# Kernel optimization log

Measured on AMD Instinct MI355X. Metric: run time of the kernel, lower is better.

Reference implementation:

```python
import jax, jax.numpy as jnp
import numpy as np

B, C, H, W = 8, 128, 128, 128
WS, NH = 4, 8
HD = C // NH
SCALE = HD ** -0.5
HG, WG = H // WS, W // WS
G, N = HG * WG, WS * WS


def conv2d(x, w, b, padding=0, groups=1):
    out = jax.lax.conv_general_dilated(
        x, w, (1, 1), [(padding, padding)] * 2,
        dimension_numbers=('NCHW', 'OIHW', 'NCHW'),
        feature_group_count=groups)
    return out + b[None, :, None, None]


def dsc(x, dw_w, dw_b, pw_w, pw_b):
    # depthwise 3x3 (groups=C) then pointwise 1x1
    h = conv2d(x, dw_w, dw_b, padding=1, groups=x.shape[1])
    return conv2d(h, pw_w, pw_b)


def _window(t):
    # (B,C,H,W) -> (B,G,NH,N,HD) exactly as torch reshape/permute
    t = t.reshape(B, NH, HD, HG, WS, WG, WS)
    return t.transpose(0, 3, 5, 1, 4, 6, 2).reshape(B, G, NH, N, HD)


def setup_inputs() -> dict:
    key = jax.random.key(0)
    ks = jax.random.split(key, 32)
    s = 0.02
    Cr = max(C // 8, 1)
    d = {
        'x': jax.random.normal(ks[0], (B, C, H, W), jnp.float32),
        'y': jax.random.normal(ks[1], (B, C, H, W), jnp.float32),
        'ca_w1': jax.random.normal(ks[2], (Cr, 2 * C, 1, 1)) * s,
        'ca_b1': jnp.zeros((Cr,)),
        'ca_w2': jax.random.normal(ks[3], (2 * C, Cr, 1, 1)) * s,
        'ca_b2': jnp.zeros((2 * C,)),
        'final_w': jax.random.normal(ks[4], (C, 3 * C, 1, 1)) * s,
        'final_b': jnp.zeros((C,)),
        'bn_g': jnp.ones((C,)),
        'bn_b': jnp.zeros((C,)),
        'bn_m': jnp.zeros((C,)),
        'bn_v': jnp.ones((C,)),
    }
    for i, name in enumerate(['q', 'k', 'v', 'proj']):
        d[name + '_dw_w'] = jax.random.normal(ks[5 + 4 * i], (C, 1, 3, 3)) * s
        d[name + '_dw_b'] = jnp.zeros((C,))
        d[name + '_pw_w'] = jax.random.normal(ks[6 + 4 * i], (C, C, 1, 1)) * s
        d[name + '_pw_b'] = jnp.zeros((C,))
    return d


def reference(x, y, ca_w1, ca_b1, ca_w2, ca_b2,
              q_dw_w, q_dw_b, q_pw_w, q_pw_b,
              k_dw_w, k_dw_b, k_pw_w, k_pw_b,
              v_dw_w, v_dw_b, v_pw_w, v_pw_b,
              proj_dw_w, proj_dw_b, proj_pw_w, proj_pw_b,
              final_w, final_b, bn_g, bn_b, bn_m, bn_v):
    element_wise = x * y
    concat = jnp.concatenate([x, y], axis=1)  # (B,2C,H,W)
    # channel attention (squeeze-excite)
    pooled = concat.mean(axis=(2, 3), keepdims=True)
    h = jax.nn.relu(conv2d(pooled, ca_w1, ca_b1))
    ca = jax.nn.sigmoid(conv2d(h, ca_w2, ca_b2))
    attended = concat * ca
    x_att, y_att = attended[:, :C], attended[:, C:]
    # windowed cross-attention: q from y_att, k/v from x_att
    q = _window(dsc(y_att, q_dw_w, q_dw_b, q_pw_w, q_pw_b))
    k = _window(dsc(x_att, k_dw_w, k_dw_b, k_pw_w, k_pw_b))
    v = _window(dsc(x_att, v_dw_w, v_dw_b, v_pw_w, v_pw_b))
    attn = jnp.einsum('bgnqd,bgnkd->bgnqk', q, k) * SCALE
    attn = jax.nn.softmax(attn, axis=-1)
    out = jnp.einsum('bgnqk,bgnkd->bgnqd', attn, v)  # (B,G,NH,N,HD)
    out = out.transpose(0, 1, 3, 2, 4).reshape(B, HG, WG, WS, WS, C)
    out = out.transpose(0, 1, 3, 2, 4, 5).reshape(B, H, W, C).transpose(0, 3, 1, 2)
    cross = dsc(out, proj_dw_w, proj_dw_b, proj_pw_w, proj_pw_b)
    fused = jnp.concatenate([element_wise, y_att, cross], axis=1)
    z = conv2d(fused, final_w, final_b)
    # BatchNorm in eval mode with running stats
    inv = jax.lax.rsqrt(bn_v + 1e-5)
    z = (z - bn_m[None, :, None, None]) * (inv * bn_g)[None, :, None, None] + bn_b[None, :, None, None]
    return jax.nn.relu(z)
```

## Files before the change

### kernel.cpp

```cpp
#include <hip/hip_runtime.h>

typedef __attribute__((ext_vector_type(8))) short short8;
typedef __attribute__((ext_vector_type(4))) float f32x4;
typedef __attribute__((ext_vector_type(2))) unsigned u32x2;
typedef __attribute__((ext_vector_type(4))) unsigned u32x4;

static constexpr int C_ = 128, H_ = 128, W_ = 128;
static constexpr int HW_ = H_ * W_;
static constexpr int CHW_ = C_ * HW_;

__device__ __forceinline__ unsigned short f2b(float f) {
  union { float f; unsigned u; } cv; cv.f = f;
  unsigned r = cv.u + 0x7FFFu + ((cv.u >> 16) & 1u);
  return (unsigned short)(r >> 16);
}
__device__ __forceinline__ float b2f(unsigned short h) {
  union { unsigned u; float f; } cv; cv.u = ((unsigned)h) << 16;
  return cv.f;
}
__device__ __forceinline__ float uasf(unsigned u) {
  union { unsigned u; float f; } cv; cv.u = u; return cv.f;
}
__device__ __forceinline__ int swzo(int pos, int byteInRow) {
  return pos * 256 + (byteInRow ^ ((pos & 7) << 4));
}

__global__ __launch_bounds__(256) void k_pool(const float* __restrict__ x,
                                              const float* __restrict__ y,
                                              float* __restrict__ sums) {
  int blk = blockIdx.x;
  int b = blk >> 8, c = blk & 255;
  const float* src = (c < C_) ? (x + (size_t)b * CHW_ + (size_t)c * HW_)
                              : (y + (size_t)b * CHW_ + (size_t)(c - C_) * HW_);
  const float4* s4 = (const float4*)src;
  float acc = 0.f;
  for (int i = threadIdx.x; i < HW_ / 4; i += 256) {
    float4 v = s4[i];
    acc += v.x + v.y + v.z + v.w;
  }
  for (int off = 32; off; off >>= 1) acc += __shfl_down(acc, off, 64);
  __shared__ float red[4];
  int lane = threadIdx.x & 63, wv = threadIdx.x >> 6;
  if (lane == 0) red[wv] = acc;
  __syncthreads();
  if (threadIdx.x == 0) sums[blk] = red[0] + red[1] + red[2] + red[3];
}

__global__ __launch_bounds__(256) void k_ca(const float* __restrict__ sums,
                                            const float* __restrict__ w1,
                                            const float* __restrict__ b1,
                                            const float* __restrict__ w2,
                                            const float* __restrict__ b2,
                                            float* __restrict__ ca) {
  int b = blockIdx.x;
  __shared__ float pooled[256];
  __shared__ float hb[16];
  int t = threadIdx.x;
  pooled[t] = sums[b * 256 + t] * (1.f / 16384.f);
  __syncthreads();
  if (t < 16) {
    float s = b1[t];
    for (int j = 0; j < 256; ++j) s += w1[t * 256 + j] * pooled[j];
    hb[t] = fmaxf(s, 0.f);
  }
  __syncthreads();
  float s = b2[t];
  for (int r = 0; r < 16; ++r) s += w2[t * 16 + r] * hb[r];
  ca[b * 256 + t] = 1.f / (1.f + __expf(-s));
}

__global__ __launch_bounds__(128) void k_prep(
    const float* __restrict__ qpw, const float* __restrict__ kpw,
    const float* __restrict__ vpw,
    const float* __restrict__ fw, const float* __restrict__ fb,
    const float* __restrict__ ppw, const float* __restrict__ ppb,
    const float* __restrict__ cab,
    unsigned short* __restrict__ Wb, unsigned short* __restrict__ W2b,
    float* __restrict__ bc) {
  int blk = blockIdx.x, c = threadIdx.x;
  if (blk < 768) {
    int mat = blk >> 7, o = blk & 127;
    float v = 0.f;
    if (mat == 0) v = qpw[o * 128 + c];
    else if (mat == 1) v = kpw[o * 128 + c];
    else if (mat == 2) v = vpw[o * 128 + c];
    else if (mat == 3) {
      float a = 0.f;
      for (int m = 0; m < 128; ++m) a += fw[o * 384 + 256 + m] * ppw[m * 128 + c];
      v = a;
      if (c == 0) {
        float bb = fb[o];
        for (int m = 0; m < 128; ++m) bb += fw[o * 384 + 256 + m] * ppb[m];
        bc[o] = bb;
      }
    } else if (mat == 4) v = fw[o * 384 + c];
    else v = 0.f;
    Wb[((size_t)mat << 14) + o * 128 + c] = f2b(v);
  } else {
    int bb = (blk - 768) >> 7, o = blk & 127;
    W2b[((size_t)bb << 14) + o * 128 + c] =
        f2b(fw[o * 384 + 128 + c] * cab[bb * 256 + 128 + c]);
  }
}

__global__ __launch_bounds__(512, 4) void k_qkv_attn(
    const float* __restrict__ x, const float* __restrict__ y,
    const float* __restrict__ cab,
    const float* __restrict__ qdw, const float* __restrict__ qdb,
    const float* __restrict__ kdw, const float* __restrict__ kdb,
    const float* __restrict__ vdw, const float* __restrict__ vdb,
    const unsigned short* __restrict__ Wqkv,
    const float* __restrict__ qpb, const float* __restrict__ kpb,
    const float* __restrict__ vpb,
    unsigned short* __restrict__ outb) {
  __shared__ __align__(16) char lds[81920];
  constexpr int QS = 0, KS = 16384, VT = 32768, A1 = 49152, A2 = 65536;
  constexpr int HA = 16384, SCR = 49152, OS = 65536;

  const int t = threadIdx.x;
  const int l = t & 63;
  const int w = t >> 6;
  const int lm = l & 15, g = l >> 4;
  const int bs = ((blockIdx.x & 7) << 8) | (blockIdx.x >> 3);
  const int b = bs >> 8, tr = bs & 255;
  const int y0 = (tr >> 3) << 2, x0 = (tr & 7) << 4;
  const int ct = t & 127, rowt = t >> 7;
  unsigned short* hal = (unsigned short*)(lds + HA);

  auto halo_issue = [&](const float* src, f32x4 (*hv)[6]) {
    #pragma unroll
    for (int tk = 0; tk < 2; ++tk) {
      int task = t + tk * 512;
      bool tv = task < 768;
      int c = task & 127, hr = task >> 7;
      int gy = y0 - 1 + hr;
      bool rowok = tv && ((unsigned)gy < 128u);
      const float* rsrc = src + (size_t)c * HW_ + gy * W_;
      #pragma unroll
      for (int ck = 0; ck < 6; ++ck) {
        int gxc = x0 - 4 + 4 * ck;
        bool ok = rowok && ((unsigned)gxc < 125u);
        hv[tk][ck] = ok ? *(const f32x4*)(rsrc + gxc) : f32x4{0.f, 0.f, 0.f, 0.f};
      }
    }
  };
  auto halo_write = [&](const f32x4 (*hv)[6]) {
    #pragma unroll
    for (int tk = 0; tk < 2; ++tk) {
      int task = t + tk * 512;
      if (task < 768) {
        int base = ((task >> 7) * 128 + (task & 127)) * 18;
        const float* f = (const float*)hv[tk];
        #pragma unroll
        for (int e = 0; e < 9; ++e) {
          unsigned u = (unsigned)f2b(f[2 * e + 3]) |
                       ((unsigned)f2b(f[2 * e + 4]) << 16);
          *(unsigned*)(hal + base + 2 * e) = u;
        }
      }
    }
  };

  auto dw_one = [&](const float* wdw, const float* bdw, const float* cas,
                    int aOff) {
    const float* wp = wdw + ct * 9;
    float wr[9];
    #pragma unroll
    for (int k2 = 0; k2 < 9; ++k2) wr[k2] = wp[k2];
    float cam = cas[ct], bb = bdw[ct];
    float o[16];
    #pragma unroll
    for (int px = 0; px < 16; ++px) o[px] = 0.f;
    #pragma unroll
    for (int rr = 0; rr < 3; ++rr) {
      int base = ((rowt + rr) * 128 + ct) * 18;
      unsigned rp[9];
      #pragma unroll
      for (int e = 0; e < 9; ++e) rp[e] = *(const unsigned*)(hal + base + 2 * e);
      float rv[18];
      #pragma unroll
      for (int e = 0; e < 9; ++e) {
        rv[2 * e] = uasf(rp[e] << 16);
        rv[2 * e + 1] = uasf(rp[e] & 0xffff0000u);
      }
      #pragma unroll
      for (int px = 0; px < 16; ++px)
        o[px] += rv[px] * wr[3 * rr] + rv[px + 1] * wr[3 * rr + 1] +
                 rv[px + 2] * wr[3 * rr + 2];
    }
    #pragma unroll
    for (int px = 0; px < 16; ++px)
      *(unsigned short*)(lds + aOff + swzo(rowt * 16 + px, 2 * ct)) =
          f2b(o[px] * cam + bb);
  };
  auto dw_kv = [&](const float* kw, const float* kb2, const float* vw,
                   const float* vb2, const float* cas) {
    const float* kp = kw + ct * 9;
    const float* vp = vw + ct * 9;
    float wk[9], wv2[9];
    #pragma unroll
    for (int k2 = 0; k2 < 9; ++k2) { wk[k2] = kp[k2]; wv2[k2] = vp[k2]; }
    float cam = cas[ct], kbb = kb2[ct], vbb = vb2[ct];
    float ok[16], ov[16];
    #pragma unroll
    for (int px = 0; px < 16; ++px) { ok[px] = 0.f; ov[px] = 0.f; }
    #pragma unroll
    for (int rr = 0; rr < 3; ++rr) {
      int base = ((rowt + rr) * 128 + ct) * 18;
      unsigned rp[9];
      #pragma unroll
      for (int e = 0; e < 9; ++e) rp[e] = *(const unsigned*)(hal + base + 2 * e);
      float rv[18];
      #pragma unroll
      for (int e = 0; e < 9; ++e) {
        rv[2 * e] = uasf(rp[e] << 16);
        rv[2 * e + 1] = uasf(rp[e] & 0xffff0000u);
      }
      #pragma unroll
      for (int px = 0; px < 16; ++px) {
        ok[px] += rv[px] * wk[3 * rr] + rv[px + 1] * wk[3 * rr + 1] +
                  rv[px + 2] * wk[3 * rr + 2];
        ov[px] += rv[px] * wv2[3 * rr] + rv[px + 1] * wv2[3 * rr + 1] +
                  rv[px + 2] * wv2[3 * rr + 2];
      }
    }
    #pragma unroll
    for (int px = 0; px < 16; ++px) {
      int so = swzo(rowt * 16 + px, 2 * ct);
      *(unsigned short*)(lds + A1 + so) = f2b(ok[px] * cam + kbb);
      *(unsigned short*)(lds + A2 + so) = f2b(ov[px] * cam + vbb);
    }
  };

  const int mtile = w & 3, nbase = (w >> 2) * 64;

  auto gemm_qk = [&](int aOff, const unsigned short* Wm, const float* bias,
                     int dstOff) {
    f32x4 acc[4];
    #pragma unroll
    for (int nt = 0; nt < 4; ++nt) acc[nt] = f32x4{0.f, 0.f, 0.f, 0.f};
    #pragma unroll
    for (int ks = 0; ks < 4; ++ks) {
      short8 wf[4];
      #pragma unroll
      for (int nt = 0; nt < 4; ++nt)
        wf[nt] = *(const short8*)(Wm + (nbase + nt * 16 + lm) * 128 +
                                  ks * 32 + g * 8);
      short8 a = *(const short8*)(lds + aOff +
                   swzo(mtile * 16 + lm, ks * 64 + g * 16));
      #pragma unroll
      for (int nt = 0; nt < 4; ++nt)
        acc[nt] = __builtin_amdgcn_mfma_f32_16x16x32_bf16(a, wf[nt], acc[nt], 0, 0, 0);
    }
    #pragma unroll
    for (int nt = 0; nt < 4; ++nt) {
      int ch = nbase + nt * 16 + lm;
      float bv = bias[ch];
      #pragma unroll
      for (int r2 = 0; r2 < 4; ++r2) {
        int pos = mtile * 16 + g * 4 + r2;
        *(unsigned short*)(lds + dstOff + swzo(pos, 2 * ch)) =
            f2b(acc[nt][r2] + bv);
      }
    }
  };
  auto gemm_v = [&](int aOff, const unsigned short* Wm, const float* bias) {
    f32x4 acc[4];
    #pragma unroll
    for (int nt = 0; nt < 4; ++nt) acc[nt] = f32x4{0.f, 0.f, 0.f, 0.f};
    #pragma unroll
    for (int ks = 0; ks < 4; ++ks) {
      short8 wf[4];
      #pragma unroll
      for (int nt = 0; nt < 4; ++nt)
        wf[nt] = *(const short8*)(Wm + (nbase + nt * 16 + lm) * 128 +
                                  ks * 32 + g * 8);
      short8 a = *(const short8*)(lds + aOff +
                   swzo(mtile * 16 + lm, ks * 64 + g * 16));
      #pragma unroll
      for (int nt = 0; nt < 4; ++nt)
        acc[nt] = __builtin_amdgcn_mfma_f32_16x16x32_bf16(a, wf[nt], acc[nt], 0, 0, 0);
    }
    #pragma unroll
    for (int nt = 0; nt < 4; ++nt) {
      int ch = nbase + nt * 16 + lm;
      float bv = bias[ch];
      int col = (g * 16 + mtile * 4) ^ ((ch & 7) << 3);
      unsigned lo = (unsigned)f2b(acc[nt][0] + bv) |
                    ((unsigned)f2b(acc[nt][1] + bv) << 16);
      unsigned hi = (unsigned)f2b(acc[nt][2] + bv) |
                    ((unsigned)f2b(acc[nt][3] + bv) << 16);
      *(u32x2*)(lds + VT + ch * 128 + 2 * col) = u32x2{lo, hi};
    }
  };

  const float* cax = cab + b * 256;
  const float* cay = cax + 128;

  f32x4 hy[2][6], hx[2][6];
  halo_issue(y + (size_t)b * CHW_, hy);
  halo_issue(x + (size_t)b * CHW_, hx);
  halo_write(hy);
  __syncthreads();
  dw_one(qdw, qdb, cay, A1);
  __syncthreads();
  halo_write(hx);
  gemm_qk(A1, Wqkv, qpb, QS);
  __syncthreads();
  dw_kv(kdw, kdb, vdw, vdb, cax);
  __syncthreads();
  gemm_qk(A1, Wqkv + 16384, kpb, KS);
  gemm_v(A2, Wqkv + 32768, vpb);
  __syncthreads();

  {
    const int h = w;
    const int chb = h * 32;
    char* scr = lds + SCR + w * 512;
    const short8 zz = {};
    #pragma unroll
    for (int wi = 0; wi < 4; ++wi) {
      int rowp = (lm >> 2) * 16 + wi * 4 + (lm & 3);
      short8 av = zz, bv = zz;
      if (g < 2) {
        av = *(const short8*)(lds + KS + swzo(rowp, chb + g * 16));
        bv = *(const short8*)(lds + QS + swzo(rowp, chb + g * 16));
      }
      f32x4 st = __builtin_amdgcn_mfma_f32_16x16x32_bf16(
          av, bv, f32x4{0.f, 0.f, 0.f, 0.f}, 0, 0, 0);
      float s0 = st[0] * 0.25f, s1 = st[1] * 0.25f,
            s2 = st[2] * 0.25f, s3 = st[3] * 0.25f;
      float mx = fmaxf(fmaxf(s0, s1), fmaxf(s2, s3));
      mx = fmaxf(mx, __shfl_xor(mx, 16, 64));
      mx = fmaxf(mx, __shfl_xor(mx, 32, 64));
      float e0 = __expf(s0 - mx), e1 = __expf(s1 - mx),
            e2 = __expf(s2 - mx), e3 = __expf(s3 - mx);
      float sm = e0 + e1 + e2 + e3;
      sm += __shfl_xor(sm, 16, 64);
      sm += __shfl_xor(sm, 32, 64);
      float rl = 1.f / sm;
      unsigned p0 = (unsigned)f2b(e0 * rl) | ((unsigned)f2b(e1 * rl) << 16);
      unsigned p1 = (unsigned)f2b(e2 * rl) | ((unsigned)f2b(e3 * rl) << 16);
      *(u32x2*)(scr + lm * 32 + g * 8) = u32x2{p0, p1};
      short8 pb2 = zz, va = zz;
      if (g < 2) {
        pb2 = *(const short8*)(scr + lm * 32 + g * 16);
        int ch = h * 16 + lm;
        va = *(const short8*)(lds + VT + ch * 128 +
                              2 * ((wi * 16 + g * 8) ^ ((ch & 7) << 3)));
      }
      f32x4 ot = __builtin_amdgcn_mfma_f32_16x16x32_bf16(
          va, pb2, f32x4{0.f, 0.f, 0.f, 0.f}, 0, 0, 0);
      unsigned o0 = (unsigned)f2b(ot[0]) | ((unsigned)f2b(ot[1]) << 16);
      unsigned o1 = (unsigned)f2b(ot[2]) | ((unsigned)f2b(ot[3]) << 16);
      *(u32x2*)(lds + OS + swzo(rowp, chb + g * 8)) = u32x2{o0, o1};
    }
  }
  __syncthreads();
  {
    unsigned short* dst = outb + (size_t)b * CHW_ + (size_t)ct * HW_ +
                          (y0 + rowt) * W_ + x0;
    unsigned v[8];
    #pragma unroll
    for (int j = 0; j < 8; ++j) {
      unsigned lo = *(const unsigned short*)(lds + OS + swzo(rowt * 16 + 2 * j, 2 * ct));
      unsigned hi = *(const unsigned short*)(lds + OS + swzo(rowt * 16 + 2 * j + 1, 2 * ct));
      v[j] = lo | (hi << 16);
    }
    *(u32x4*)(dst) = u32x4{v[0], v[1], v[2], v[3]};
    *(u32x4*)(dst + 8) = u32x4{v[4], v[5], v[6], v[7]};
  }
}

__global__ __launch_bounds__(512, 4) void k_final(
    const float* __restrict__ x, const float* __restrict__ y,
    const unsigned short* __restrict__ outb,
    const float* __restrict__ pdw, const float* __restrict__ pdb,
    const unsigned short* __restrict__ W3,
    const unsigned short* __restrict__ W2b,
    const float* __restrict__ bc,
    const float* __restrict__ bng, const float* __restrict__ bnb,
    const float* __restrict__ bnm, const float* __restrict__ bnv,
    float* __restrict__ outp) {
  __shared__ __align__(16) char lds[50176];
  constexpr int A1 = 0, HA = 16384;

  const int t = threadIdx.x, l = t & 63, w = t >> 6;
  const int lm = l & 15, g = l >> 4;
  const int bs = ((blockIdx.x & 7) << 8) | (blockIdx.x >> 3);
  const int b = bs >> 8, tr = bs & 255;
  const int y0 = (tr >> 3) << 2, x0 = (tr & 7) << 4;
  const int ct = t & 127, rowt = t >> 7;
  unsigned short* hal = (unsigned short*)(lds + HA);
  const int mtile = w & 3, nbase = (w >> 2) * 64;

  f32x4 acc[4];
  #pragma unroll
  for (int nt = 0; nt < 4; ++nt) acc[nt] = f32x4{0.f, 0.f, 0.f, 0.f};

  auto gemm_acc = [&](const unsigned short* Wm) {
    #pragma unroll
    for (int ks = 0; ks < 4; ++ks) {
      short8 wf[4];
      #pragma unroll
      for (int nt = 0; nt < 4; ++nt)
        wf[nt] = *(const short8*)(Wm + (nbase + nt * 16 + lm) * 128 +
                                  ks * 32 + g * 8);
      short8 a = *(const short8*)(lds + A1 +
                   swzo(mtile * 16 + lm, ks * 64 + g * 16));
      #pragma unroll
      for (int nt = 0; nt < 4; ++nt)
        acc[nt] = __builtin_amdgcn_mfma_f32_16x16x32_bf16(a, wf[nt], acc[nt], 0, 0, 0);
    }
  };

  const size_t gbase = (size_t)b * CHW_ + (size_t)ct * HW_ +
                       (size_t)(y0 + rowt) * W_ + x0;
  f32x4 xv[4], yv[4];
  #pragma unroll
  for (int e = 0; e < 4; ++e) {
    xv[e] = *(const f32x4*)(x + gbase + 4 * e);
    yv[e] = *(const f32x4*)(y + gbase + 4 * e);
  }
  unsigned hreg[2][10];
  #pragma unroll
  for (int tk = 0; tk < 2; ++tk) {
    int task = t + tk * 512;
    bool tv = task < 768;
    int c = task & 127, hr = task >> 7;
    int gy = y0 - 1 + hr;
    bool rowok = tv && ((unsigned)gy < 128u);
    const unsigned short* hsrc = outb + (size_t)b * CHW_ + (size_t)c * HW_ + gy * W_;
    #pragma unroll
    for (int e = 0; e < 10; ++e) {
      int gx0 = x0 - 2 + 2 * e;
      bool okp = rowok && ((unsigned)gx0 < 127u);
      hreg[tk][e] = okp ? *(const unsigned*)(hsrc + gx0) : 0u;
    }
  }
  #pragma unroll
  for (int e = 0; e < 4; ++e)
    #pragma unroll
    for (int j = 0; j < 4; ++j)
      *(unsigned short*)(lds + A1 + swzo(rowt * 16 + 4 * e + j, 2 * ct)) =
          f2b(xv[e][j] * yv[e][j]);
  #pragma unroll
  for (int tk = 0; tk < 2; ++tk) {
    int task = t + tk * 512;
    if (task < 768) {
      int base = ((task >> 7) * 128 + (task & 127)) * 22;
      #pragma unroll
      for (int e = 0; e < 10; ++e)
        *(unsigned*)(hal + base + 2 * e) = hreg[tk][e];
    }
  }
  __syncthreads();
  gemm_acc(W3 + 16384);
  __syncthreads();
  #pragma unroll
  for (int e = 0; e < 4; ++e)
    #pragma unroll
    for (int j = 0; j < 4; ++j)
      *(unsigned short*)(lds + A1 + swzo(rowt * 16 + 4 * e + j, 2 * ct)) =
          f2b(yv[e][j]);
  __syncthreads();
  gemm_acc(W2b + ((size_t)b << 14));
  __syncthreads();
  {
    const float* wp = pdw + ct * 9;
    float wr[9];
    #pragma unroll
    for (int k2 = 0; k2 < 9; ++k2) wr[k2] = wp[k2];
    float bb = pdb[ct];
    float o[16];
    #pragma unroll
    for (int px = 0; px < 16; ++px) o[px] = 0.f;
    #pragma unroll
    for (int rr = 0; rr < 3; ++rr) {
      int base = ((rowt + rr) * 128 + ct) * 22;
      unsigned rp[10];
      #pragma unroll
      for (int e = 0; e < 10; ++e) rp[e] = *(const unsigned*)(hal + base + 2 * e);
      float rv[20];
      #pragma unroll
      for (int e = 0; e < 10; ++e) {
        rv[2 * e] = uasf(rp[e] << 16);
        rv[2 * e + 1] = uasf(rp[e] & 0xffff0000u);
      }
      #pragma unroll
      for (int px = 0; px < 16; ++px)
        o[px] += rv[px + 1] * wr[3 * rr] + rv[px + 2] * wr[3 * rr + 1] +
                 rv[px + 3] * wr[3 * rr + 2];
    }
    #pragma unroll
    for (int px = 0; px < 16; ++px)
      *(unsigned short*)(lds + A1 + swzo(rowt * 16 + px, 2 * ct)) =
          f2b(o[px] + bb);
  }
  __syncthreads();
  gemm_acc(W3);
  float* fst = (float*)(lds + HA);
  #pragma unroll
  for (int nt = 0; nt < 4; ++nt) {
    int ch = nbase + nt * 16 + lm;
    float zb = bc[ch];
    float inv = rsqrtf(bnv[ch] + 1e-5f);
    float gsc = inv * bng[ch];
    float mm = bnm[ch], ab = bnb[ch];
    #pragma unroll
    for (int r2 = 0; r2 < 4; ++r2) {
      int pos = mtile * 16 + g * 4 + r2;
      float z = acc[nt][r2] + zb;
      z = (z - mm) * gsc + ab;
      fst[pos * 130 + ch] = fmaxf(z, 0.f);
    }
  }
  __syncthreads();
  #pragma unroll
  for (int e4 = 0; e4 < 4; ++e4) {
    f32x4 ov;
    #pragma unroll
    for (int j = 0; j < 4; ++j) ov[j] = fst[(rowt * 16 + e4 * 4 + j) * 130 + ct];
    *(f32x4*)(outp + gbase + 4 * e4) = ov;
  }
}

extern "C" void kernel_launch(void* const* d_in, const int* in_sizes, int n_in,
                              void* d_out, int out_size, void* d_ws, size_t ws_size,
                              hipStream_t stream) {
  const float* x       = (const float*)d_in[0];
  const float* y       = (const float*)d_in[1];
  const float* ca_w1   = (const float*)d_in[2];
  const float* ca_b1   = (const float*)d_in[3];
  const float* ca_w2   = (const float*)d_in[4];
  const float* ca_b2   = (const float*)d_in[5];
  const float* final_w = (const float*)d_in[6];
  const float* final_b = (const float*)d_in[7];
  const float* bn_g    = (const float*)d_in[8];
  const float* bn_b    = (const float*)d_in[9];
  const float* bn_m    = (const float*)d_in[10];
  const float* bn_v    = (const float*)d_in[11];
  const float* q_dw_w  = (const float*)d_in[12];
  const float* q_dw_b  = (const float*)d_in[13];
  const float* q_pw_w  = (const float*)d_in[14];
  const float* q_pw_b  = (const float*)d_in[15];
  const float* k_dw_w  = (const float*)d_in[16];
  const float* k_dw_b  = (const float*)d_in[17];
  const float* k_pw_w  = (const float*)d_in[18];
  const float* k_pw_b  = (const float*)d_in[19];
  const float* v_dw_w  = (const float*)d_in[20];
  const float* v_dw_b  = (const float*)d_in[21];
  const float* v_pw_w  = (const float*)d_in[22];
  const float* v_pw_b  = (const float*)d_in[23];
  const float* p_dw_w  = (const float*)d_in[24];
  const float* p_dw_b  = (const float*)d_in[25];
  const float* p_pw_w  = (const float*)d_in[26];
  const float* p_pw_b  = (const float*)d_in[27];

  char* ws = (char*)d_ws;
  float* sums = (float*)(ws + 0);
  float* cab  = (float*)(ws + 8192);
  unsigned short* Wqkv = (unsigned short*)(ws + 16384);
  unsigned short* W3   = Wqkv + 3 * 16384;
  float* bc   = (float*)(ws + 212992);
  unsigned short* W2b  = (unsigned short*)(ws + 213504);
  unsigned short* outb = (unsigned short*)(ws + (1 << 20));

  k_pool<<<2048, 256, 0, stream>>>(x, y, sums);
  k_ca<<<8, 256, 0, stream>>>(sums, ca_w1, ca_b1, ca_w2, ca_b2, cab);
  k_prep<<<1792, 128, 0, stream>>>(q_pw_w, k_pw_w, v_pw_w, final_w, final_b,
                                   p_pw_w, p_pw_b, cab, Wqkv, W2b, bc);
  k_qkv_attn<<<2048, 512, 0, stream>>>(x, y, cab,
      q_dw_w, q_dw_b, k_dw_w, k_dw_b, v_dw_w, v_dw_b,
      Wqkv, q_pw_b, k_pw_b, v_pw_b, outb);
  k_final<<<2048, 512, 0, stream>>>(x, y, outb,
      p_dw_w, p_dw_b, W3, W2b, bc,
      bn_g, bn_b, bn_m, bn_v, (float*)d_out);
}
```

Measured before the change: 360.9 us.

## Drop LDS halo staging and reuse LDS buffers to raise occupancy

The depthwise convolutions in the QKV-attention kernel now read their 3x3 neighbourhoods straight from global memory into registers instead of staging a bf16 halo tile in LDS. A-fragments are loaded into registers so the GEMM outputs can overwrite their own source buffers, and the attention output is held in registers until all waves finish. Together these shrink LDS from 80KB to 52KB, and launch bounds are raised to 6 waves per SIMD on both kernels. The cost is redundant global or L2 reads (each row is fetched three times), losing the overlap of x and y halo loads, extra barriers, and tighter register limits that may cause spills.

```diff
diff --git a/kernel.cpp b/kernel.cpp
--- a/kernel.cpp
+++ b/kernel.cpp
@@ -103,7 +103,7 @@
   }
 }
 
-__global__ __launch_bounds__(512, 4) void k_qkv_attn(
+__global__ __launch_bounds__(512, 6) void k_qkv_attn(
     const float* __restrict__ x, const float* __restrict__ y,
     const float* __restrict__ cab,
     const float* __restrict__ qdw, const float* __restrict__ qdb,
@@ -113,9 +113,11 @@
     const float* __restrict__ qpb, const float* __restrict__ kpb,
     const float* __restrict__ vpb,
     unsigned short* __restrict__ outb) {
-  __shared__ __align__(16) char lds[81920];
-  constexpr int QS = 0, KS = 16384, VT = 32768, A1 = 49152, A2 = 65536;
-  constexpr int HA = 16384, SCR = 49152, OS = 65536;
+  __shared__ __align__(16) char lds[53248];
+  constexpr int QS = 0, OS = 0;
+  constexpr int AK = 16384, KS = 16384;
+  constexpr int AV = 32768, VT = 32768;
+  constexpr int SCR = 49152;
 
   const int t = threadIdx.x;
   const int l = t & 63;
@@ -125,117 +127,85 @@
   const int b = bs >> 8, tr = bs & 255;
   const int y0 = (tr >> 3) << 2, x0 = (tr & 7) << 4;
   const int ct = t & 127, rowt = t >> 7;
-  unsigned short* hal = (unsigned short*)(lds + HA);
-
-  auto halo_issue = [&](const float* src, f32x4 (*hv)[6]) {
-    #pragma unroll
-    for (int tk = 0; tk < 2; ++tk) {
-      int task = t + tk * 512;
-      bool tv = task < 768;
-      int c = task & 127, hr = task >> 7;
-      int gy = y0 - 1 + hr;
-      bool rowok = tv && ((unsigned)gy < 128u);
-      const float* rsrc = src + (size_t)c * HW_ + gy * W_;
+  const int mtile = w & 3, nbase = (w >> 2) * 64;
+
+  auto dw_direct = [&](const float* src, const float* wdw,
+                       const float* bdw, const float* cas, int aOff) {
+    const float* wp = wdw + ct * 9;
+    const float* rbase = src + (size_t)ct * HW_;
+    float o[16];
+    #pragma unroll
+    for (int px = 0; px < 16; ++px) o[px] = 0.f;
+    #pragma unroll
+    for (int rr = 0; rr < 3; ++rr) {
+      int gy = y0 + rowt - 1 + rr;
+      bool rowok = (unsigned)gy < 128u;
+      f32x4 rx[6];
       #pragma unroll
       for (int ck = 0; ck < 6; ++ck) {
-        int gxc = x0 - 4 + 4 * ck;
-        bool ok = rowok && ((unsigned)gxc < 125u);
-        hv[tk][ck] = ok ? *(const f32x4*)(rsrc + gxc) : f32x4{0.f, 0.f, 0.f, 0.f};
-      }
-    }
-  };
-  auto halo_write = [&](const f32x4 (*hv)[6]) {
-    #pragma unroll
-    for (int tk = 0; tk < 2; ++tk) {
-      int task = t + tk * 512;
-      if (task < 768) {
-        int base = ((task >> 7) * 128 + (task & 127)) * 18;
-        const float* f = (const float*)hv[tk];
-        #pragma unroll
-        for (int e = 0; e < 9; ++e) {
-          unsigned u = (unsigned)f2b(f[2 * e + 3]) |
-                       ((unsigned)f2b(f[2 * e + 4]) << 16);
-          *(unsigned*)(hal + base + 2 * e) = u;
-        }
-      }
-    }
-  };
-
-  auto dw_one = [&](const float* wdw, const float* bdw, const float* cas,
-                    int aOff) {
-    const float* wp = wdw + ct * 9;
-    float wr[9];
-    #pragma unroll
-    for (int k2 = 0; k2 < 9; ++k2) wr[k2] = wp[k2];
+        int gx0 = x0 - 4 + 4 * ck;
+        bool ok2 = rowok && ((unsigned)gx0 < 125u);
+        rx[ck] = ok2 ? *(const f32x4*)(rbase + (size_t)gy * W_ + gx0)
+                     : f32x4{0.f, 0.f, 0.f, 0.f};
+      }
+      float w0 = wp[3 * rr], w1 = wp[3 * rr + 1], w2 = wp[3 * rr + 2];
+      const float* f = (const float*)rx;
+      #pragma unroll
+      for (int px = 0; px < 16; ++px)
+        o[px] += f[px + 3] * w0 + f[px + 4] * w1 + f[px + 5] * w2;
+    }
     float cam = cas[ct], bb = bdw[ct];
-    float o[16];
-    #pragma unroll
-    for (int px = 0; px < 16; ++px) o[px] = 0.f;
-    #pragma unroll
-    for (int rr = 0; rr < 3; ++rr) {
-      int base = ((rowt + rr) * 128 + ct) * 18;
-      unsigned rp[9];
-      #pragma unroll
-      for (int e = 0; e < 9; ++e) rp[e] = *(const unsigned*)(hal + base + 2 * e);
-      float rv[18];
-      #pragma unroll
-      for (int e = 0; e < 9; ++e) {
-        rv[2 * e] = uasf(rp[e] << 16);
-        rv[2 * e + 1] = uasf(rp[e] & 0xffff0000u);
-      }
-      #pragma unroll
-      for (int px = 0; px < 16; ++px)
-        o[px] += rv[px] * wr[3 * rr] + rv[px + 1] * wr[3 * rr + 1] +
-                 rv[px + 2] * wr[3 * rr + 2];
-    }
     #pragma unroll
     for (int px = 0; px < 16; ++px)
       *(unsigned short*)(lds + aOff + swzo(rowt * 16 + px, 2 * ct)) =
           f2b(o[px] * cam + bb);
   };
-  auto dw_kv = [&](const float* kw, const float* kb2, const float* vw,
-                   const float* vb2, const float* cas) {
+  auto dw_kv_direct = [&](const float* src, const float* kw, const float* kb2,
+                          const float* vw, const float* vb2, const float* cas) {
     const float* kp = kw + ct * 9;
     const float* vp = vw + ct * 9;
-    float wk[9], wv2[9];
-    #pragma unroll
-    for (int k2 = 0; k2 < 9; ++k2) { wk[k2] = kp[k2]; wv2[k2] = vp[k2]; }
+    const float* rbase = src + (size_t)ct * HW_;
+    float ok[16], ov[16];
+    #pragma unroll
+    for (int px = 0; px < 16; ++px) { ok[px] = 0.f; ov[px] = 0.f; }
+    #pragma unroll
+    for (int rr = 0; rr < 3; ++rr) {
+      int gy = y0 + rowt - 1 + rr;
+      bool rowok = (unsigned)gy < 128u;
+      f32x4 rx[6];
+      #pragma unroll
+      for (int ck = 0; ck < 6; ++ck) {
+        int gx0 = x0 - 4 + 4 * ck;
+        bool ok2 = rowok && ((unsigned)gx0 < 125u);
+        rx[ck] = ok2 ? *(const f32x4*)(rbase + (size_t)gy * W_ + gx0)
+                     : f32x4{0.f, 0.f, 0.f, 0.f};
+      }
+      float k0 = kp[3 * rr], k1 = kp[3 * rr + 1], k2 = kp[3 * rr + 2];
+      float v0 = vp[3 * rr], v1 = vp[3 * rr + 1], v2 = vp[3 * rr + 2];
+      const float* f = (const float*)rx;
+      #pragma unroll
+      for (int px = 0; px < 16; ++px) {
+        ok[px] += f[px + 3] * k0 + f[px + 4] * k1 + f[px + 5] * k2;
+        ov[px] += f[px + 3] * v0 + f[px + 4] * v1 + f[px + 5] * v2;
+      }
+    }
     float cam = cas[ct], kbb = kb2[ct], vbb = vb2[ct];
-    float ok[16], ov[16];
-    #pragma unroll
-    for (int px = 0; px < 16; ++px) { ok[px] = 0.f; ov[px] = 0.f; }
-    #pragma unroll
-    for (int rr = 0; rr < 3; ++rr) {
-      int base = ((rowt + rr) * 128 + ct) * 18;
-      unsigned rp[9];
-      #pragma unroll
-      for (int e = 0; e < 9; ++e) rp[e] = *(const unsigned*)(hal + base + 2 * e);
-      float rv[18];
-      #pragma unroll
-      for (int e = 0; e < 9; ++e) {
-        rv[2 * e] = uasf(rp[e] << 16);
-        rv[2 * e + 1] = uasf(rp[e] & 0xffff0000u);
-      }
-      #pragma unroll
-      for (int px = 0; px < 16; ++px) {
-        ok[px] += rv[px] * wk[3 * rr] + rv[px + 1] * wk[3 * rr + 1] +
-                  rv[px + 2] * wk[3 * rr + 2];
-        ov[px] += rv[px] * wv2[3 * rr] + rv[px + 1] * wv2[3 * rr + 1] +
-                  rv[px + 2] * wv2[3 * rr + 2];
-      }
-    }
     #pragma unroll
     for (int px = 0; px < 16; ++px) {
       int so = swzo(rowt * 16 + px, 2 * ct);
-      *(unsigned short*)(lds + A1 + so) = f2b(ok[px] * cam + kbb);
-      *(unsigned short*)(lds + A2 + so) = f2b(ov[px] * cam + vbb);
+      *(unsigned short*)(lds + AK + so) = f2b(ok[px] * cam + kbb);
+      *(unsigned short*)(lds + AV + so) = f2b(ov[px] * cam + vbb);
     }
   };
 
-  const int mtile = w & 3, nbase = (w >> 2) * 64;
-
-  auto gemm_qk = [&](int aOff, const unsigned short* Wm, const float* bias,
-                     int dstOff) {
+  auto afrag_load = [&](int aOff, short8* a) {
+    #pragma unroll
+    for (int ks = 0; ks < 4; ++ks)
+      a[ks] = *(const short8*)(lds + aOff +
+                 swzo(mtile * 16 + lm, ks * 64 + g * 16));
+  };
+  auto gemm_from = [&](const short8* a, const unsigned short* Wm,
+                       const float* bias, int dstOff) {
     f32x4 acc[4];
     #pragma unroll
     for (int nt = 0; nt < 4; ++nt) acc[nt] = f32x4{0.f, 0.f, 0.f, 0.f};
@@ -246,11 +216,9 @@
       for (int nt = 0; nt < 4; ++nt)
         wf[nt] = *(const short8*)(Wm + (nbase + nt * 16 + lm) * 128 +
                                   ks * 32 + g * 8);
-      short8 a = *(const short8*)(lds + aOff +
-                   swzo(mtile * 16 + lm, ks * 64 + g * 16));
       #pragma unroll
       for (int nt = 0; nt < 4; ++nt)
-        acc[nt] = __builtin_amdgcn_mfma_f32_16x16x32_bf16(a, wf[nt], acc[nt], 0, 0, 0);
+        acc[nt] = __builtin_amdgcn_mfma_f32_16x16x32_bf16(a[ks], wf[nt], acc[nt], 0, 0, 0);
     }
     #pragma unroll
     for (int nt = 0; nt < 4; ++nt) {
@@ -264,7 +232,8 @@
       }
     }
   };
-  auto gemm_v = [&](int aOff, const unsigned short* Wm, const float* bias) {
+  auto gemm_v_from = [&](const short8* a, const unsigned short* Wm,
+                         const float* bias) {
     f32x4 acc[4];
     #pragma unroll
     for (int nt = 0; nt < 4; ++nt) acc[nt] = f32x4{0.f, 0.f, 0.f, 0.f};
@@ -275,11 +244,9 @@
       for (int nt = 0; nt < 4; ++nt)
         wf[nt] = *(const short8*)(Wm + (nbase + nt * 16 + lm) * 128 +
                                   ks * 32 + g * 8);
-      short8 a = *(const short8*)(lds + aOff +
-                   swzo(mtile * 16 + lm, ks * 64 + g * 16));
       #pragma unroll
       for (int nt = 0; nt < 4; ++nt)
-        acc[nt] = __builtin_amdgcn_mfma_f32_16x16x32_bf16(a, wf[nt], acc[nt], 0, 0, 0);
+        acc[nt] = __builtin_amdgcn_mfma_f32_16x16x32_bf16(a[ks], wf[nt], acc[nt], 0, 0, 0);
     }
     #pragma unroll
     for (int nt = 0; nt < 4; ++nt) {
@@ -296,23 +263,27 @@
 
   const float* cax = cab + b * 256;
   const float* cay = cax + 128;
-
-  f32x4 hy[2][6], hx[2][6];
-  halo_issue(y + (size_t)b * CHW_, hy);
-  halo_issue(x + (size_t)b * CHW_, hx);
-  halo_write(hy);
-  __syncthreads();
-  dw_one(qdw, qdb, cay, A1);
-  __syncthreads();
-  halo_write(hx);
-  gemm_qk(A1, Wqkv, qpb, QS);
-  __syncthreads();
-  dw_kv(kdw, kdb, vdw, vdb, cax);
-  __syncthreads();
-  gemm_qk(A1, Wqkv + 16384, kpb, KS);
-  gemm_v(A2, Wqkv + 32768, vpb);
-  __syncthreads();
-
+  const float* xb = x + (size_t)b * CHW_;
+  const float* yb = y + (size_t)b * CHW_;
+
+  dw_direct(yb, qdw, qdb, cay, QS);
+  __syncthreads();
+  short8 aq[4];
+  afrag_load(QS, aq);
+  __syncthreads();
+  gemm_from(aq, Wqkv, qpb, QS);
+  __builtin_amdgcn_sched_barrier(0);
+  dw_kv_direct(xb, kdw, kdb, vdw, vdb, cax);
+  __syncthreads();
+  short8 ak[4], av[4];
+  afrag_load(AK, ak);
+  afrag_load(AV, av);
+  __syncthreads();
+  gemm_from(ak, Wqkv + 16384, kpb, KS);
+  gemm_v_from(av, Wqkv + 32768, vpb);
+  __syncthreads();
+
+  u32x2 oac[4];
   {
     const int h = w;
     const int chb = h * 32;
@@ -321,13 +292,13 @@
     #pragma unroll
     for (int wi = 0; wi < 4; ++wi) {
       int rowp = (lm >> 2) * 16 + wi * 4 + (lm & 3);
-      short8 av = zz, bv = zz;
+      short8 avf = zz, bvf = zz;
       if (g < 2) {
-        av = *(const short8*)(lds + KS + swzo(rowp, chb + g * 16));
-        bv = *(const short8*)(lds + QS + swzo(rowp, chb + g * 16));
+        avf = *(const short8*)(lds + KS + swzo(rowp, chb + g * 16));
+        bvf = *(const short8*)(lds + QS + swzo(rowp, chb + g * 16));
       }
       f32x4 st = __builtin_amdgcn_mfma_f32_16x16x32_bf16(
-          av, bv, f32x4{0.f, 0.f, 0.f, 0.f}, 0, 0, 0);
+          avf, bvf, f32x4{0.f, 0.f, 0.f, 0.f}, 0, 0, 0);
       float s0 = st[0] * 0.25f, s1 = st[1] * 0.25f,
             s2 = st[2] * 0.25f, s3 = st[3] * 0.25f;
       float mx = fmaxf(fmaxf(s0, s1), fmaxf(s2, s3));
@@ -353,7 +324,16 @@
           va, pb2, f32x4{0.f, 0.f, 0.f, 0.f}, 0, 0, 0);
       unsigned o0 = (unsigned)f2b(ot[0]) | ((unsigned)f2b(ot[1]) << 16);
       unsigned o1 = (unsigned)f2b(ot[2]) | ((unsigned)f2b(ot[3]) << 16);
-      *(u32x2*)(lds + OS + swzo(rowp, chb + g * 8)) = u32x2{o0, o1};
+      oac[wi] = u32x2{o0, o1};
+    }
+  }
+  __syncthreads();
+  {
+    const int chb = w * 32;
+    #pragma unroll
+    for (int wi = 0; wi < 4; ++wi) {
+      int rowp = (lm >> 2) * 16 + wi * 4 + (lm & 3);
+      *(u32x2*)(lds + OS + swzo(rowp, chb + g * 8)) = oac[wi];
     }
   }
   __syncthreads();
@@ -372,7 +352,7 @@
   }
 }
 
-__global__ __launch_bounds__(512, 4) void k_final(
+__global__ __launch_bounds__(512, 6) void k_final(
     const float* __restrict__ x, const float* __restrict__ y,
     const unsigned short* __restrict__ outb,
     const float* __restrict__ pdw, const float* __restrict__ pdb,
```

After: 516.6 us. 43.1% more time.

## Emit bf16 x*y and y copies from attention kernel for final stage

Applied to the files above, without the earlier changes.

The attention kernel already loads x and y halos, so it now also writes bf16 copies of y and of the elementwise product x*y to workspace buffers. A new final kernel reads these bf16 tensors instead of re-reading fp32 x and y. This halves the final kernel's input traffic for those operands, at the cost of extra writes in the attention kernel and extra workspace. The old path is kept as a fallback when the workspace is too small.

```diff
diff --git a/kernel.cpp b/kernel.cpp
--- a/kernel.cpp
+++ b/kernel.cpp
@@ -13,10 +13,6 @@
   union { float f; unsigned u; } cv; cv.f = f;
   unsigned r = cv.u + 0x7FFFu + ((cv.u >> 16) & 1u);
   return (unsigned short)(r >> 16);
-}
-__device__ __forceinline__ float b2f(unsigned short h) {
-  union { unsigned u; float f; } cv; cv.u = ((unsigned)h) << 16;
-  return cv.f;
 }
 __device__ __forceinline__ float uasf(unsigned u) {
   union { unsigned u; float f; } cv; cv.u = u; return cv.f;
@@ -103,6 +99,7 @@
   }
 }
 
+template <int EM>
 __global__ __launch_bounds__(512, 4) void k_qkv_attn(
     const float* __restrict__ x, const float* __restrict__ y,
     const float* __restrict__ cab,
@@ -112,7 +109,9 @@
     const unsigned short* __restrict__ Wqkv,
     const float* __restrict__ qpb, const float* __restrict__ kpb,
     const float* __restrict__ vpb,
-    unsigned short* __restrict__ outb) {
+    unsigned short* __restrict__ outb,
+    unsigned short* __restrict__ emb,
+    unsigned short* __restrict__ ybb) {
   __shared__ __align__(16) char lds[81920];
   constexpr int QS = 0, KS = 16384, VT = 32768, A1 = 49152, A2 = 65536;
   constexpr int HA = 16384, SCR = 49152, OS = 65536;
@@ -301,10 +300,31 @@
   halo_issue(y + (size_t)b * CHW_, hy);
   halo_issue(x + (size_t)b * CHW_, hx);
   halo_write(hy);
+  const int itk = (t < 128) ? 1 : 0;
+  const int itask = t + itk * 512;
+  const int ic = itask & 127, ihr = itask >> 7;
+  unsigned py_[8];
+  if (EM) {
+    const float* fy = (const float*)hy[itk];
+    #pragma unroll
+    for (int e = 0; e < 8; ++e)
+      py_[e] = (unsigned)f2b(fy[4 + 2 * e]) |
+               ((unsigned)f2b(fy[5 + 2 * e]) << 16);
+  }
   __syncthreads();
   dw_one(qdw, qdb, cay, A1);
   __syncthreads();
   halo_write(hx);
+  unsigned pe_[8];
+  if (EM) {
+    const float* fx = (const float*)hx[itk];
+    #pragma unroll
+    for (int e = 0; e < 8; ++e) {
+      float ya = uasf(py_[e] << 16), yb2 = uasf(py_[e] & 0xffff0000u);
+      pe_[e] = (unsigned)f2b(fx[4 + 2 * e] * ya) |
+               ((unsigned)f2b(fx[5 + 2 * e] * yb2) << 16);
+    }
+  }
   gemm_qk(A1, Wqkv, qpb, QS);
   __syncthreads();
   dw_kv(kdw, kdb, vdw, vdb, cax);
@@ -321,13 +341,13 @@
     #pragma unroll
     for (int wi = 0; wi < 4; ++wi) {
       int rowp = (lm >> 2) * 16 + wi * 4 + (lm & 3);
-      short8 av = zz, bv = zz;
+      short8 avf = zz, bvf = zz;
       if (g < 2) {
-        av = *(const short8*)(lds + KS + swzo(rowp, chb + g * 16));
-        bv = *(const short8*)(lds + QS + swzo(rowp, chb + g * 16));
+        avf = *(const short8*)(lds + KS + swzo(rowp, chb + g * 16));
+        bvf = *(const short8*)(lds + QS + swzo(rowp, chb + g * 16));
       }
       f32x4 st = __builtin_amdgcn_mfma_f32_16x16x32_bf16(
-          av, bv, f32x4{0.f, 0.f, 0.f, 0.f}, 0, 0, 0);
+          avf, bvf, f32x4{0.f, 0.f, 0.f, 0.f}, 0, 0, 0);
       float s0 = st[0] * 0.25f, s1 = st[1] * 0.25f,
             s2 = st[2] * 0.25f, s3 = st[3] * 0.25f;
       float mx = fmaxf(fmaxf(s0, s1), fmaxf(s2, s3));
@@ -370,9 +390,180 @@
     *(u32x4*)(dst) = u32x4{v[0], v[1], v[2], v[3]};
     *(u32x4*)(dst + 8) = u32x4{v[4], v[5], v[6], v[7]};
   }
-}
-
-__global__ __launch_bounds__(512, 4) void k_final(
+  if (EM) {
+    size_t off = (size_t)b * CHW_ + (size_t)ic * HW_ +
+                 (size_t)(y0 + ihr - 1) * W_ + x0;
+    *(u32x4*)(ybb + off) = u32x4{py_[0], py_[1], py_[2], py_[3]};
+    *(u32x4*)(ybb + off + 8) = u32x4{py_[4], py_[5], py_[6], py_[7]};
+    *(u32x4*)(emb + off) = u32x4{pe_[0], pe_[1], pe_[2], pe_[3]};
+    *(u32x4*)(emb + off + 8) = u32x4{pe_[4], pe_[5], pe_[6], pe_[7]};
+  }
+}
+
+__global__ __launch_bounds__(512, 4) void k_final_em(
+    const unsigned short* __restrict__ emb,
+    const unsigned short* __restrict__ ybb,
+    const unsigned short* __restrict__ outb,
+    const float* __restrict__ pdw, const float* __restrict__ pdb,
+    const unsigned short* __restrict__ W3,
+    const unsigned short* __restrict__ W2b,
+    const float* __restrict__ bc,
+    const float* __restrict__ bng, const float* __restrict__ bnb,
+    const float* __restrict__ bnm, const float* __restrict__ bnv,
+    float* __restrict__ outp) {
+  __shared__ __align__(16) char lds[50176];
+  constexpr int A1 = 0, HA = 16384;
+
+  const int t = threadIdx.x, l = t & 63, w = t >> 6;
+  const int lm = l & 15, g = l >> 4;
+  const int bs = ((blockIdx.x & 7) << 8) | (blockIdx.x >> 3);
+  const int b = bs >> 8, tr = bs & 255;
+  const int y0 = (tr >> 3) << 2, x0 = (tr & 7) << 4;
+  const int ct = t & 127, rowt = t >> 7;
+  unsigned short* hal = (unsigned short*)(lds + HA);
+  const int mtile = w & 3, nbase = (w >> 2) * 64;
+
+  f32x4 acc[4];
+  #pragma unroll
+  for (int nt = 0; nt < 4; ++nt) acc[nt] = f32x4{0.f, 0.f, 0.f, 0.f};
+
+  auto gemm_acc = [&](const unsigned short* Wm) {
+    #pragma unroll
+    for (int ks = 0; ks < 4; ++ks) {
+      short8 wf[4];
+      #pragma unroll
+      for (int nt = 0; nt < 4; ++nt)
+        wf[nt] = *(const short8*)(Wm + (nbase + nt * 16 + lm) * 128 +
+                                  ks * 32 + g * 8);
+      short8 a = *(const short8*)(lds + A1 +
+                   swzo(mtile * 16 + lm, ks * 64 + g * 16));
+      #pragma unroll
+      for (int nt = 0; nt < 4; ++nt)
+        acc[nt] = __builtin_amdgcn_mfma_f32_16x16x32_bf16(a, wf[nt], acc[nt], 0, 0, 0);
+    }
+  };
+
+  const size_t rowoff = (size_t)b * CHW_ + (size_t)ct * HW_ +
+                        (size_t)(y0 + rowt) * W_ + x0;
+
+  unsigned hreg[2][10];
+  #pragma unroll
+  for (int tk = 0; tk < 2; ++tk) {
+    int task = t + tk * 512;
+    bool tv = task < 768;
+    int c = task & 127, hr = task >> 7;
+    int gy = y0 - 1 + hr;
+    bool rowok = tv && ((unsigned)gy < 128u);
+    const unsigned short* hsrc = outb + (size_t)b * CHW_ + (size_t)c * HW_ + gy * W_;
+    #pragma unroll
+    for (int e = 0; e < 10; ++e) {
+      int gx0 = x0 - 2 + 2 * e;
+      bool okp = rowok && ((unsigned)gx0 < 127u);
+      hreg[tk][e] = okp ? *(const unsigned*)(hsrc + gx0) : 0u;
+    }
+  }
+  u32x4 em0 = *(const u32x4*)(emb + rowoff);
+  u32x4 em1 = *(const u32x4*)(emb + rowoff + 8);
+  u32x4 yr0 = *(const u32x4*)(ybb + rowoff);
+  u32x4 yr1 = *(const u32x4*)(ybb + rowoff + 8);
+  #pragma unroll
+  for (int e = 0; e < 4; ++e) {
+    *(unsigned short*)(lds + A1 + swzo(rowt * 16 + 2 * e, 2 * ct)) =
+        (unsigned short)em0[e];
+    *(unsigned short*)(lds + A1 + swzo(rowt * 16 + 2 * e + 1, 2 * ct)) =
+        (unsigned short)(em0[e] >> 16);
+    *(unsigned short*)(lds + A1 + swzo(rowt * 16 + 8 + 2 * e, 2 * ct)) =
+        (unsigned short)em1[e];
+    *(unsigned short*)(lds + A1 + swzo(rowt * 16 + 8 + 2 * e + 1, 2 * ct)) =
+        (unsigned short)(em1[e] >> 16);
+  }
+  #pragma unroll
+  for (int tk = 0; tk < 2; ++tk) {
+    int task = t + tk * 512;
+    if (task < 768) {
+      int base = ((task >> 7) * 128 + (task & 127)) * 22;
+      #pragma unroll
+      for (int e = 0; e < 10; ++e)
+        *(unsigned*)(hal + base + 2 * e) = hreg[tk][e];
+    }
+  }
+  __syncthreads();
+  gemm_acc(W3 + 16384);
+  __syncthreads();
+  #pragma unroll
+  for (int e = 0; e < 4; ++e) {
+    *(unsigned short*)(lds + A1 + swzo(rowt * 16 + 2 * e, 2 * ct)) =
+        (unsigned short)yr0[e];
+    *(unsigned short*)(lds + A1 + swzo(rowt * 16 + 2 * e + 1, 2 * ct)) =
+        (unsigned short)(yr0[e] >> 16);
+    *(unsigned short*)(lds + A1 + swzo(rowt * 16 + 8 + 2 * e, 2 * ct)) =
+        (unsigned short)yr1[e];
+    *(unsigned short*)(lds + A1 + swzo(rowt * 16 + 8 + 2 * e + 1, 2 * ct)) =
+        (unsigned short)(yr1[e] >> 16);
+  }
+  __syncthreads();
+  gemm_acc(W2b + ((size_t)b << 14));
+  __syncthreads();
+  {
+    const float* wp = pdw + ct * 9;
+    float wr[9];
+    #pragma unroll
+    for (int k2 = 0; k2 < 9; ++k2) wr[k2] = wp[k2];
+    float bb = pdb[ct];
+    float o[16];
+    #pragma unroll
+    for (int px = 0; px < 16; ++px) o[px] = 0.f;
+    #pragma unroll
+    for (int rr = 0; rr < 3; ++rr) {
+      int base = ((rowt + rr) * 128 + ct) * 22;
+      unsigned rp[10];
+      #pragma unroll
+      for (int e = 0; e < 10; ++e) rp[e] = *(const unsigned*)(hal + base + 2 * e);
+      float rv[20];
+      #pragma unroll
+      for (int e = 0; e < 10; ++e) {
+        rv[2 * e] = uasf(rp[e] << 16);
+        rv[2 * e + 1] = uasf(rp[e] & 0xffff0000u);
+      }
+      #pragma unroll
+      for (int px = 0; px < 16; ++px)
+        o[px] += rv[px + 1] * wr[3 * rr] + rv[px + 2] * wr[3 * rr + 1] +
+                 rv[px + 3] * wr[3 * rr + 2];
+    }
+    #pragma unroll
+    for (int px = 0; px < 16; ++px)
+      *(unsigned short*)(lds + A1 + swzo(rowt * 16 + px, 2 * ct)) =
+          f2b(o[px] + bb);
+  }
+  __syncthreads();
+  gemm_acc(W3);
+  float* fst = (float*)(lds + HA);
+  #pragma unroll
+  for (int nt = 0; nt < 4; ++nt) {
+    int ch = nbase + nt * 16 + lm;
+    float zb = bc[ch];
+    float inv = rsqrtf(bnv[ch] + 1e-5f);
+    float gsc = inv * bng[ch];
+    float mm = bnm[ch], ab = bnb[ch];
+    #pragma unroll
+    for (int r2 = 0; r2 < 4; ++r2) {
+      int pos = mtile * 16 + g * 4 + r2;
+      float z = acc[nt][r2] + zb;
+      z = (z - mm) * gsc + ab;
+      fst[pos * 130 + ch] = fmaxf(z, 0.f);
+    }
+  }
+  __syncthreads();
+  #pragma unroll
+  for (int e4 = 0; e4 < 4; ++e4) {
+    f32x4 ov;
+    #pragma unroll
+    for (int j = 0; j < 4; ++j) ov[j] = fst[(rowt * 16 + e4 * 4 + j) * 130 + ct];
+    *(f32x4*)(outp + rowoff + 4 * e4) = ov;
+  }
+}
+
+__global__ __launch_bounds__(512, 4) void k_final_xy(
     const float* __restrict__ x, const float* __restrict__ y,
     const unsigned short* __restrict__ outb,
     const float* __restrict__ pdw, const float* __restrict__ pdb,
@@ -564,16 +755,29 @@
   unsigned short* W3   = Wqkv + 3 * 16384;
   float* bc   = (float*)(ws + 212992);
   unsigned short* W2b  = (unsigned short*)(ws + 213504);
+  constexpr size_t BUF = 33554432ull;
   unsigned short* outb = (unsigned short*)(ws + (1 << 20));
+  unsigned short* emb  = (unsigned short*)(ws + (1 << 20) + BUF);
+  unsigned short* ybb  = (unsigned short*)(ws + (1 << 20) + 2 * BUF);
+  const bool em_ok = ws_size >= (size_t)(1 << 20) + 3 * BUF;
 
   k_pool<<<2048, 256, 0, stream>>>(x, y, sums);
   k_ca<<<8, 256, 0, stream>>>(sums, ca_w1, ca_b1, ca_w2, ca_b2, cab);
   k_prep<<<1792, 128, 0, stream>>>(q_pw_w, k_pw_w, v_pw_w, final_w, final_b,
                                    p_pw_w, p_pw_b, cab, Wqkv, W2b, bc);
-  k_qkv_attn<<<2048, 512, 0, stream>>>(x, y, cab,
-      q_dw_w, q_dw_b, k_dw_w, k_dw_b, v_dw_w, v_dw_b,
-      Wqkv, q_pw_b, k_pw_b, v_pw_b, outb);
-  k_final<<<2048, 512, 0, stream>>>(x, y, outb,
-      p_dw_w, p_dw_b, W3, W2b, bc,
-      bn_g, bn_b, bn_m, bn_v, (float*)d_out);
-}
+  if (em_ok) {
+    k_qkv_attn<1><<<2048, 512, 0, stream>>>(x, y, cab,
+        q_dw_w, q_dw_b, k_dw_w, k_dw_b, v_dw_w, v_dw_b,
+        Wqkv, q_pw_b, k_pw_b, v_pw_b, outb, emb, ybb);
+    k_final_em<<<2048, 512, 0, stream>>>(emb, ybb, outb,
+        p_dw_w, p_dw_b, W3, W2b, bc,
+        bn_g, bn_b, bn_m, bn_v, (float*)d_out);
+  } else {
+    k_qkv_attn<0><<<2048, 512, 0, stream>>>(x, y, cab,
+        q_dw_w, q_dw_b, k_dw_w, k_dw_b, v_dw_w, v_dw_b,
+        Wqkv, q_pw_b, k_pw_b, v_pw_b, outb, outb, outb);
+    k_final_xy<<<2048, 512, 0, stream>>>(x, y, outb,
+        p_dw_w, p_dw_b, W3, W2b, bc,
+        bn_g, bn_b, bn_m, bn_v, (float*)d_out);
+  }
+}
```

Measured after the change: 482.9 us. 33.8% more time.
